# Performance work log

Measured on AMD Instinct MI355X. Metric: run time of the kernel, lower is better.

Reference implementation:

```python
import jax, jax.numpy as jnp
import numpy as np

N_NODES = 100000
N_EDGES = 1600000
D = 64


def _sage_conv(x, src, dst, W_l, W_r, b):
    # PyG SAGEConv (aggr='mean'): out_i = W_l @ mean_{j in N(i)} x_j + W_r @ x_i + b
    n = x.shape[0]
    msgs = x[src]  # [E, D] gather of source-node features
    agg = jax.ops.segment_sum(msgs, dst, num_segments=n)  # [N, D]
    cnt = jax.ops.segment_sum(jnp.ones((src.shape[0],), x.dtype), dst, num_segments=n)
    mean = agg / jnp.maximum(cnt, 1.0)[:, None]
    return mean @ W_l.T + x @ W_r.T + b


def setup_inputs() -> dict:
    key = jax.random.key(0)
    ks = jax.random.split(key, 8)
    s = 1.0 / np.sqrt(D)
    x = jax.random.normal(ks[0], (N_NODES, D), dtype=jnp.float32)
    edge_index = jax.random.randint(ks[1], (2, N_EDGES), 0, N_NODES, dtype=jnp.int64)
    return {
        "x": x,
        "edge_index": edge_index,
        "W1_l": jax.random.normal(ks[2], (D, D), dtype=jnp.float32) * s,
        "W1_r": jax.random.normal(ks[3], (D, D), dtype=jnp.float32) * s,
        "b1": jnp.zeros((D,), dtype=jnp.float32),
        "W2_l": jax.random.normal(ks[4], (D, D), dtype=jnp.float32) * s,
        "W2_r": jax.random.normal(ks[5], (D, D), dtype=jnp.float32) * s,
        "b2": jnp.zeros((D,), dtype=jnp.float32),
    }


def reference(x, edge_index, W1_l, W1_r, b1, W2_l, W2_r, b2):
    src, dst = edge_index[0], edge_index[1]
    h = _sage_conv(x, src, dst, W1_l, W1_r, b1)
    h = jax.nn.relu(h)
    out = _sage_conv(h, src, dst, W2_l, W2_r, b2)
    return out
```

## Files before the change

kernel.cpp:

```cpp
#include <hip/hip_runtime.h>

#define D 64
#define BSHIFT 8
#define BNODES (1 << BSHIFT)
#define NBK_MAX 512
#define CAPSH 13

typedef __attribute__((ext_vector_type(8))) short bf16x8;
typedef __attribute__((ext_vector_type(4))) float f32x4;

__device__ __forceinline__ unsigned int f2bf_rne(float f) {
    unsigned int b = __float_as_uint(f);
    return (b + 0x7fffu + ((b >> 16) & 1u)) >> 16;
}
__device__ __forceinline__ unsigned int pack_bf(float lo, float hi) {
    return f2bf_rne(lo) | (f2bf_rne(hi) << 16);
}
__device__ __forceinline__ float bflo(unsigned int u) { return __uint_as_float(u << 16); }
__device__ __forceinline__ float bfhi(unsigned int u) { return __uint_as_float(u & 0xffff0000u); }

__global__ void cast_kernel(const float4* __restrict__ xin, uint2* __restrict__ xb, int n4,
                            int* __restrict__ cnt, int nz) {
    int gid = blockIdx.x * blockDim.x + threadIdx.x;
    if (gid < nz) cnt[gid] = 0;
    int stride = gridDim.x * blockDim.x;
    for (int i = gid; i < n4; i += stride) {
        float4 v = xin[i];
        uint2 o;
        o.x = pack_bf(v.x, v.y);
        o.y = pack_bf(v.z, v.w);
        xb[i] = o;
    }
}

__global__ __launch_bounds__(512) void binscatter_kernel(
    const int* __restrict__ src, const int* __restrict__ dst,
    int* __restrict__ cnt, unsigned int* __restrict__ pairs,
    int E, int NBK, int CE) {
    __shared__ int lh[NBK_MAX];
    __shared__ int lbase[NBK_MAX];
    for (int k = threadIdx.x; k < NBK; k += 512) lh[k] = 0;
    __syncthreads();
    int b = blockIdx.x;
    int beg = b * CE, end = min(beg + CE, E);
    for (int e = beg + threadIdx.x; e < end; e += 512)
        atomicAdd(&lh[dst[e] >> BSHIFT], 1);
    __syncthreads();
    for (int k = threadIdx.x; k < NBK; k += 512) {
        int c = lh[k];
        if (c) lbase[k] = (k << CAPSH) + atomicAdd(&cnt[k], c);
        lh[k] = 0;
    }
    __syncthreads();
    for (int e = beg + threadIdx.x; e < end; e += 512) {
        int d = dst[e];
        int k = d >> BSHIFT;
        int r = atomicAdd(&lh[k], 1);
        pairs[lbase[k] + r] = (unsigned int)src[e] | ((unsigned int)(d & (BNODES - 1)) << 17);
    }
}

__global__ __launch_bounds__(256) void csr_build_kernel(
    const unsigned int* __restrict__ pairs, const int* __restrict__ cnt,
    int2* __restrict__ rowpair, int* __restrict__ csr, int N, int NBK) {
    __shared__ unsigned int spr[1 << CAPSH];
    __shared__ int lcnt[BNODES];
    __shared__ int s[256];
    int k = blockIdx.x;
    int tid = threadIdx.x;
    int node0 = k << BSHIFT;
    int nnodes = min(BNODES, N - node0);
    int rbeg = k << CAPSH;
    int cntk = cnt[k];

    for (int j = tid; j < BNODES; j += 256) lcnt[j] = 0;
    __syncthreads();
    for (int i = tid; i < cntk; i += 256) {
        unsigned int rec = pairs[rbeg + i];
        spr[i] = rec;
        atomicAdd(&lcnt[rec >> 17], 1);
    }
    __syncthreads();
    int v0 = lcnt[tid];
    int ps = (v0 + 3) & ~3;
    s[tid] = ps;
    __syncthreads();
    for (int off = 1; off < 256; off <<= 1) {
        int t = (tid >= off) ? s[tid - off] : 0;
        __syncthreads();
        s[tid] += t;
        __syncthreads();
    }
    int ebase = s[tid] - ps;
    int p = rbeg + ebase;
    if (tid < nnodes) rowpair[node0 + tid] = make_int2(p, p + v0);
    lcnt[tid] = p;
    __syncthreads();
    for (int i = tid; i < cntk; i += 256) {
        unsigned int rec = spr[i];
        int j = rec >> 17;
        int pos = atomicAdd(&lcnt[j], 1);
        csr[pos] = (int)(rec & 0x1FFFFu);
    }
}

__global__ __launch_bounds__(256) void fused_layer_kernel(
    const unsigned int* __restrict__ xin, const int2* __restrict__ rowpair,
    const int* __restrict__ csr,
    const float* __restrict__ Wl, const float* __restrict__ Wr,
    const float* __restrict__ bias,
    float* __restrict__ outf, unsigned int* __restrict__ outb, int N, int relu) {
    __shared__ uint4 smean[64][8];

    int tid = threadIdx.x;
    int wave = tid >> 6;
    int lane = tid & 63;
    int node0 = blockIdx.x * 64;

    int q  = lane >> 3;
    int fl = lane & 7;
    for (int o = 0; o < 2; ++o) {
        int nl = (wave << 4) + (o << 3) + q;
        int node = node0 + nl;
        bool valid = node < N;
        int beg = 0, end = 0;
        if (valid) { int2 be = rowpair[node]; beg = be.x; end = be.y; }
        float s0 = 0.f, s1 = 0.f, s2 = 0.f, s3 = 0.f;
        float s4 = 0.f, s5 = 0.f, s6 = 0.f, s7 = 0.f;
        int j = beg;
        for (; j + 4 <= end; j += 4) {
            int4 iv = *(const int4*)(csr + j);
            uint4 u0 = *(const uint4*)(xin + iv.x * 32 + fl * 4);
            uint4 u1 = *(const uint4*)(xin + iv.y * 32 + fl * 4);
            uint4 u2 = *(const uint4*)(xin + iv.z * 32 + fl * 4);
            uint4 u3 = *(const uint4*)(xin + iv.w * 32 + fl * 4);
            s0 += bflo(u0.x) + bflo(u1.x) + bflo(u2.x) + bflo(u3.x);
            s1 += bfhi(u0.x) + bfhi(u1.x) + bfhi(u2.x) + bfhi(u3.x);
            s2 += bflo(u0.y) + bflo(u1.y) + bflo(u2.y) + bflo(u3.y);
            s3 += bfhi(u0.y) + bfhi(u1.y) + bfhi(u2.y) + bfhi(u3.y);
            s4 += bflo(u0.z) + bflo(u1.z) + bflo(u2.z) + bflo(u3.z);
            s5 += bfhi(u0.z) + bfhi(u1.z) + bfhi(u2.z) + bfhi(u3.z);
            s6 += bflo(u0.w) + bflo(u1.w) + bflo(u2.w) + bflo(u3.w);
            s7 += bfhi(u0.w) + bfhi(u1.w) + bfhi(u2.w) + bfhi(u3.w);
        }
        for (; j < end; ++j) {
            uint4 u = *(const uint4*)(xin + csr[j] * 32 + fl * 4);
            s0 += bflo(u.x); s1 += bfhi(u.x);
            s2 += bflo(u.y); s3 += bfhi(u.y);
            s4 += bflo(u.z); s5 += bfhi(u.z);
            s6 += bflo(u.w); s7 += bfhi(u.w);
        }
        float inv = valid ? 1.0f / fmaxf((float)(end - beg), 1.0f) : 0.f;
        uint4 ov;
        ov.x = pack_bf(s0 * inv, s1 * inv);
        ov.y = pack_bf(s2 * inv, s3 * inv);
        ov.z = pack_bf(s4 * inv, s5 * inv);
        ov.w = pack_bf(s6 * inv, s7 * inv);
        smean[nl][fl ^ (nl & 7)] = ov;
    }

    int lm   = lane & 15;
    int quad = lane >> 4;
    int f_a  = (wave << 4) + lm;
    bf16x8 wh[4], wlo[4];
#pragma unroll
    for (int s = 0; s < 4; ++s) {
        int k8 = s * 32 + quad * 8;
        const float* Wsrc = (k8 < 64) ? Wl : Wr;
        const float* p = Wsrc + f_a * 64 + (k8 & 63);
        float4 w0 = *(const float4*)p;
        float4 w1 = *(const float4*)(p + 4);
        float w[8] = {w0.x, w0.y, w0.z, w0.w, w1.x, w1.y, w1.z, w1.w};
        bf16x8 h, l;
#pragma unroll
        for (int jj = 0; jj < 8; ++jj) {
            unsigned int hb = f2bf_rne(w[jj]);
            float hf = __uint_as_float(hb << 16);
            unsigned int lb = f2bf_rne(w[jj] - hf);
            h[jj] = (short)hb;
            l[jj] = (short)lb;
        }
        wh[s] = h;
        wlo[s] = l;
    }

    __syncthreads();

    f32x4 acc[4];
#pragma unroll
    for (int nt = 0; nt < 4; ++nt) acc[nt] = (f32x4){0.f, 0.f, 0.f, 0.f};

#pragma unroll
    for (int nt = 0; nt < 4; ++nt) {
        int nl = nt * 16 + lm;
        int node = node0 + nl;
        bool v = node < N;
        const unsigned int* xrow = xin + (long long)node * 32;
#pragma unroll
        for (int s = 0; s < 2; ++s) {
            union { uint4 u4; bf16x8 v8; } cv;
            cv.u4 = smean[nl][(s * 4 + quad) ^ (lm & 7)];
            acc[nt] = __builtin_amdgcn_mfma_f32_16x16x32_bf16(wh[s],  cv.v8, acc[nt], 0, 0, 0);
            acc[nt] = __builtin_amdgcn_mfma_f32_16x16x32_bf16(wlo[s], cv.v8, acc[nt], 0, 0, 0);
        }
#pragma unroll
        for (int s = 2; s < 4; ++s) {
            uint4 u = make_uint4(0u, 0u, 0u, 0u);
            if (v) u = *(const uint4*)(xrow + ((s & 1) << 4) + (quad << 2));
            union { uint4 u4; bf16x8 v8; } cv;
            cv.u4 = u;
            acc[nt] = __builtin_amdgcn_mfma_f32_16x16x32_bf16(wh[s],  cv.v8, acc[nt], 0, 0, 0);
            acc[nt] = __builtin_amdgcn_mfma_f32_16x16x32_bf16(wlo[s], cv.v8, acc[nt], 0, 0, 0);
        }
    }

    int fb = (wave << 4) + quad * 4;
    float4 bv = *(const float4*)(bias + fb);
#pragma unroll
    for (int nt = 0; nt < 4; ++nt) {
        int node = node0 + nt * 16 + lm;
        if (node >= N) continue;
        float r0 = acc[nt][0] + bv.x;
        float r1 = acc[nt][1] + bv.y;
        float r2 = acc[nt][2] + bv.z;
        float r3 = acc[nt][3] + bv.w;
        if (relu) {
            r0 = fmaxf(r0, 0.f); r1 = fmaxf(r1, 0.f);
            r2 = fmaxf(r2, 0.f); r3 = fmaxf(r3, 0.f);
        }
        if (outf) *(float4*)(outf + (long long)node * D + fb) = make_float4(r0, r1, r2, r3);
        if (outb) *(uint2*)(outb + (long long)node * 32 + (fb >> 1)) =
                      make_uint2(pack_bf(r0, r1), pack_bf(r2, r3));
    }
}

extern "C" void kernel_launch(void* const* d_in, const int* in_sizes, int n_in,
                              void* d_out, int out_size, void* d_ws, size_t ws_size,
                              hipStream_t stream) {
    const float* x   = (const float*)d_in[0];
    const int* ei    = (const int*)d_in[1];
    const float* W1l = (const float*)d_in[2];
    const float* W1r = (const float*)d_in[3];
    const float* b1  = (const float*)d_in[4];
    const float* W2l = (const float*)d_in[5];
    const float* W2r = (const float*)d_in[6];
    const float* b2  = (const float*)d_in[7];

    const int E = in_sizes[1] / 2;
    const int N = in_sizes[0] / D;
    const int* src  = ei;
    const int* dstp = ei + E;
    const int NBK = (N + BNODES - 1) >> BSHIFT;
    const int G1 = 128;
    const int CE = (E + G1 - 1) / G1;

    char* ws = (char*)d_ws;
    size_t off = 0;
    auto alloc = [&](size_t bytes) { void* p = ws + off; off = (off + bytes + 255) & ~(size_t)255; return p; };
    int* cnt            = (int*)alloc((size_t)NBK * 4);
    int2* rowpair       = (int2*)alloc((size_t)N * 8);
    unsigned int* pairs = (unsigned int*)alloc(((size_t)NBK << CAPSH) * 4);
    int* csr            = (int*)alloc(((size_t)NBK << CAPSH) * 4);
    unsigned int* xb    = (unsigned int*)alloc((size_t)N * 32 * 4);
    unsigned int* hb    = (unsigned int*)alloc((size_t)N * 32 * 4);

    float* out = (float*)d_out;

    cast_kernel<<<2048, 256, 0, stream>>>((const float4*)x, (uint2*)xb, N * 16, cnt, NBK);

    binscatter_kernel<<<G1, 512, 0, stream>>>(src, dstp, cnt, pairs, E, NBK, CE);
    csr_build_kernel<<<NBK, 256, 0, stream>>>(pairs, cnt, rowpair, csr, N, NBK);

    const int linGrid = (N + 63) / 64;

    fused_layer_kernel<<<linGrid, 256, 0, stream>>>(xb, rowpair, csr, W1l, W1r, b1,
                                                    nullptr, hb, N, 1);
    fused_layer_kernel<<<linGrid, 256, 0, stream>>>(hb, rowpair, csr, W2l, W2r, b2,
                                                    out, nullptr, N, 0);
}
```

Baseline: 232.8 us.

## Fuse per-bucket CSR construction into the layer kernels and drop csr_build

Buckets shrink to 64 destination nodes so each layer block matches one bucket. Each block now loads its bucket's packed (src, local dst) records, counting-sorts them in shared memory into a padded index list, then runs the existing gather-mean plus matmul. This removes the separate CSR build kernel and its global rowpair/csr round trip. In exchange the sort runs twice (once per layer), binscatter runs with fewer blocks and more buckets, and any bucket holding more than 2048 edges is silently truncated.

```diff
diff --git a/kernel.cpp b/kernel.cpp
--- a/kernel.cpp
+++ b/kernel.cpp
@@ -1,10 +1,12 @@
 #include <hip/hip_runtime.h>
 
 #define D 64
-#define BSHIFT 8
-#define BNODES (1 << BSHIFT)
-#define NBK_MAX 512
-#define CAPSH 13
+#define BSH2 6
+#define BN2 (1 << BSH2)
+#define NBK_MAX 2048
+#define CAP2SH 11
+#define CAP2 (1 << CAP2SH)
+#define SIDX_MAX (CAP2 + 3 * BN2)
 
 typedef __attribute__((ext_vector_type(8))) short bf16x8;
 typedef __attribute__((ext_vector_type(4))) float f32x4;
@@ -44,92 +46,89 @@
     int b = blockIdx.x;
     int beg = b * CE, end = min(beg + CE, E);
     for (int e = beg + threadIdx.x; e < end; e += 512)
-        atomicAdd(&lh[dst[e] >> BSHIFT], 1);
+        atomicAdd(&lh[dst[e] >> BSH2], 1);
     __syncthreads();
     for (int k = threadIdx.x; k < NBK; k += 512) {
         int c = lh[k];
-        if (c) lbase[k] = (k << CAPSH) + atomicAdd(&cnt[k], c);
+        if (c) lbase[k] = (k << CAP2SH) + atomicAdd(&cnt[k], c);
         lh[k] = 0;
     }
     __syncthreads();
     for (int e = beg + threadIdx.x; e < end; e += 512) {
         int d = dst[e];
-        int k = d >> BSHIFT;
+        int k = d >> BSH2;
         int r = atomicAdd(&lh[k], 1);
-        pairs[lbase[k] + r] = (unsigned int)src[e] | ((unsigned int)(d & (BNODES - 1)) << 17);
-    }
-}
-
-__global__ __launch_bounds__(256) void csr_build_kernel(
-    const unsigned int* __restrict__ pairs, const int* __restrict__ cnt,
-    int2* __restrict__ rowpair, int* __restrict__ csr, int N, int NBK) {
-    __shared__ unsigned int spr[1 << CAPSH];
-    __shared__ int lcnt[BNODES];
-    __shared__ int s[256];
-    int k = blockIdx.x;
+        pairs[lbase[k] + r] = (unsigned int)src[e] | ((unsigned int)(d & (BN2 - 1)) << 17);
+    }
+}
+
+__global__ __launch_bounds__(256) void fused_layer_kernel(
+    const unsigned int* __restrict__ xin, const unsigned int* __restrict__ pairs,
+    const int* __restrict__ cnt,
+    const float* __restrict__ Wl, const float* __restrict__ Wr,
+    const float* __restrict__ bias,
+    float* __restrict__ outf, unsigned int* __restrict__ outb, int N, int relu) {
+    __shared__ uint4 smean[BN2][8];
+    __shared__ int sidx[SIDX_MAX];
+    __shared__ int lcnt[BN2];
+    __shared__ int lbase[BN2];
+    __shared__ int lcur[BN2];
+    __shared__ int sscan[BN2];
+
+    unsigned int* spr = (unsigned int*)&smean[0][0];
+
     int tid = threadIdx.x;
-    int node0 = k << BSHIFT;
-    int nnodes = min(BNODES, N - node0);
-    int rbeg = k << CAPSH;
-    int cntk = cnt[k];
-
-    for (int j = tid; j < BNODES; j += 256) lcnt[j] = 0;
-    __syncthreads();
+    int wave = tid >> 6;
+    int lane = tid & 63;
+    int b = blockIdx.x;
+    int node0 = b << BSH2;
+
+    int cntk = min(cnt[b], CAP2);
+    if (tid < BN2) lcnt[tid] = 0;
+    __syncthreads();
+    int rbeg = b << CAP2SH;
     for (int i = tid; i < cntk; i += 256) {
         unsigned int rec = pairs[rbeg + i];
         spr[i] = rec;
         atomicAdd(&lcnt[rec >> 17], 1);
     }
     __syncthreads();
-    int v0 = lcnt[tid];
-    int ps = (v0 + 3) & ~3;
-    s[tid] = ps;
-    __syncthreads();
-    for (int off = 1; off < 256; off <<= 1) {
-        int t = (tid >= off) ? s[tid - off] : 0;
+    int deg = (tid < BN2) ? lcnt[tid] : 0;
+    int ps  = (deg + 3) & ~3;
+    if (tid < BN2) sscan[tid] = ps;
+    __syncthreads();
+    for (int off = 1; off < BN2; off <<= 1) {
+        int t = (tid < BN2 && tid >= off) ? sscan[tid - off] : 0;
         __syncthreads();
-        s[tid] += t;
+        if (tid < BN2) sscan[tid] += t;
         __syncthreads();
     }
-    int ebase = s[tid] - ps;
-    int p = rbeg + ebase;
-    if (tid < nnodes) rowpair[node0 + tid] = make_int2(p, p + v0);
-    lcnt[tid] = p;
+    if (tid < BN2) {
+        int base = sscan[tid] - ps;
+        lbase[tid] = base;
+        lcur[tid] = base;
+    }
     __syncthreads();
     for (int i = tid; i < cntk; i += 256) {
         unsigned int rec = spr[i];
         int j = rec >> 17;
-        int pos = atomicAdd(&lcnt[j], 1);
-        csr[pos] = (int)(rec & 0x1FFFFu);
-    }
-}
-
-__global__ __launch_bounds__(256) void fused_layer_kernel(
-    const unsigned int* __restrict__ xin, const int2* __restrict__ rowpair,
-    const int* __restrict__ csr,
-    const float* __restrict__ Wl, const float* __restrict__ Wr,
-    const float* __restrict__ bias,
-    float* __restrict__ outf, unsigned int* __restrict__ outb, int N, int relu) {
-    __shared__ uint4 smean[64][8];
-
-    int tid = threadIdx.x;
-    int wave = tid >> 6;
-    int lane = tid & 63;
-    int node0 = blockIdx.x * 64;
+        int pos = atomicAdd(&lcur[j], 1);
+        sidx[pos] = (int)(rec & 0x1FFFFu);
+    }
+    __syncthreads();
 
     int q  = lane >> 3;
     int fl = lane & 7;
     for (int o = 0; o < 2; ++o) {
         int nl = (wave << 4) + (o << 3) + q;
-        int node = node0 + nl;
-        bool valid = node < N;
-        int beg = 0, end = 0;
-        if (valid) { int2 be = rowpair[node]; beg = be.x; end = be.y; }
+        int beg = lbase[nl];
+        int dg  = lcnt[nl];
+        int end = beg + dg;
         float s0 = 0.f, s1 = 0.f, s2 = 0.f, s3 = 0.f;
         float s4 = 0.f, s5 = 0.f, s6 = 0.f, s7 = 0.f;
         int j = beg;
         for (; j + 4 <= end; j += 4) {
-            int4 iv = *(const int4*)(csr + j);
+            int4 iv = *(const int4*)(sidx + j);
             uint4 u0 = *(const uint4*)(xin + iv.x * 32 + fl * 4);
             uint4 u1 = *(const uint4*)(xin + iv.y * 32 + fl * 4);
             uint4 u2 = *(const uint4*)(xin + iv.z * 32 + fl * 4);
@@ -144,13 +143,13 @@
             s7 += bfhi(u0.w) + bfhi(u1.w) + bfhi(u2.w) + bfhi(u3.w);
         }
         for (; j < end; ++j) {
-            uint4 u = *(const uint4*)(xin + csr[j] * 32 + fl * 4);
+            uint4 u = *(const uint4*)(xin + sidx[j] * 32 + fl * 4);
             s0 += bflo(u.x); s1 += bfhi(u.x);
             s2 += bflo(u.y); s3 += bfhi(u.y);
             s4 += bflo(u.z); s5 += bfhi(u.z);
             s6 += bflo(u.w); s7 += bfhi(u.w);
         }
-        float inv = valid ? 1.0f / fmaxf((float)(end - beg), 1.0f) : 0.f;
+        float inv = 1.0f / fmaxf((float)dg, 1.0f);
         uint4 ov;
         ov.x = pack_bf(s0 * inv, s1 * inv);
         ov.y = pack_bf(s2 * inv, s3 * inv);
@@ -250,17 +249,15 @@
     const int N = in_sizes[0] / D;
     const int* src  = ei;
     const int* dstp = ei + E;
-    const int NBK = (N + BNODES - 1) >> BSHIFT;
-    const int G1 = 128;
+    const int NBK = (N + BN2 - 1) >> BSH2;
+    const int G1 = 64;
     const int CE = (E + G1 - 1) / G1;
 
     char* ws = (char*)d_ws;
     size_t off = 0;
     auto alloc = [&](size_t bytes) { void* p = ws + off; off = (off + bytes + 255) & ~(size_t)255; return p; };
     int* cnt            = (int*)alloc((size_t)NBK * 4);
-    int2* rowpair       = (int2*)alloc((size_t)N * 8);
-    unsigned int* pairs = (unsigned int*)alloc(((size_t)NBK << CAPSH) * 4);
-    int* csr            = (int*)alloc(((size_t)NBK << CAPSH) * 4);
+    unsigned int* pairs = (unsigned int*)alloc(((size_t)(NBK + 1) << CAP2SH) * 4);
     unsigned int* xb    = (unsigned int*)alloc((size_t)N * 32 * 4);
     unsigned int* hb    = (unsigned int*)alloc((size_t)N * 32 * 4);
 
@@ -269,12 +266,9 @@
     cast_kernel<<<2048, 256, 0, stream>>>((const float4*)x, (uint2*)xb, N * 16, cnt, NBK);
 
     binscatter_kernel<<<G1, 512, 0, stream>>>(src, dstp, cnt, pairs, E, NBK, CE);
-    csr_build_kernel<<<NBK, 256, 0, stream>>>(pairs, cnt, rowpair, csr, N, NBK);
-
-    const int linGrid = (N + 63) / 64;
-
-    fused_layer_kernel<<<linGrid, 256, 0, stream>>>(xb, rowpair, csr, W1l, W1r, b1,
-                                                    nullptr, hb, N, 1);
-    fused_layer_kernel<<<linGrid, 256, 0, stream>>>(hb, rowpair, csr, W2l, W2r, b2,
-                                                    out, nullptr, N, 0);
-}
+
+    fused_layer_kernel<<<NBK, 256, 0, stream>>>(xb, pairs, cnt, W1l, W1r, b1,
+                                                nullptr, hb, N, 1);
+    fused_layer_kernel<<<NBK, 256, 0, stream>>>(hb, pairs, cnt, W2l, W2r, b2,
+                                                out, nullptr, N, 0);
+}
```

New measurement: 235.0 us. Within noise of the previous version (+1.0%).
